# Optimization experiments

Measured on AMD Instinct MI355X. Metric: run time of the kernel, lower is better.

The kernel has to match this reference:

```python
import jax, jax.numpy as jnp
import numpy as np

B, N, C = 8, 4096, 256
HEADS = 8
DH = C // HEADS
SR = 4
EPS = 1e-5


def setup_inputs() -> dict:
    key = jax.random.key(0)
    ks = jax.random.split(key, 12)
    s = 0.02
    inp = {
        "x": jax.random.normal(ks[0], (B, N, C), dtype=jnp.float32),
        "H": 64,
        "W": 64,
        # nn.Linear weights stored torch-style [out, in]
        "q_w": jax.random.normal(ks[1], (C, C), dtype=jnp.float32) * s,
        "q_b": jax.random.normal(ks[2], (C,), dtype=jnp.float32) * s,
        "kv_w": jax.random.normal(ks[3], (2 * C, C), dtype=jnp.float32) * s,
        "kv_b": jax.random.normal(ks[4], (2 * C,), dtype=jnp.float32) * s,
        # Conv2d weight torch OIHW [C, C, SR, SR]
        "sr_w": jax.random.normal(ks[5], (C, C, SR, SR), dtype=jnp.float32) * s,
        "sr_b": jax.random.normal(ks[6], (C,), dtype=jnp.float32) * s,
        "ln_g": jnp.ones((C,), dtype=jnp.float32),
        "ln_b": jnp.zeros((C,), dtype=jnp.float32),
        "proj_w": jax.random.normal(ks[7], (C, C), dtype=jnp.float32) * s,
        "proj_b": jax.random.normal(ks[8], (C,), dtype=jnp.float32) * s,
    }
    return inp


def _layernorm(x, g, b):
    mu = jnp.mean(x, axis=-1, keepdims=True)
    var = jnp.mean(jnp.square(x - mu), axis=-1, keepdims=True)
    return (x - mu) * jax.lax.rsqrt(var + EPS) * g + b


def reference(x, H, W, q_w, q_b, kv_w, kv_b, sr_w, sr_b, ln_g, ln_b, proj_w, proj_b):
    b, n, c = x.shape
    scale = 1.0 / jnp.sqrt(jnp.float32(DH))

    # q projection -> [b, heads, n, dh]
    q = (x @ q_w.T + q_b).reshape(b, n, HEADS, DH).transpose(0, 2, 1, 3)

    # spatial reduction: conv stride=SR kernel=SR on the [b,H,W,c] image
    x_img = x.reshape(b, H, W, c)  # NHWC
    kern = jnp.transpose(sr_w, (2, 3, 1, 0))  # OIHW -> HWIO
    x_sr = jax.lax.conv_general_dilated(
        x_img, kern, window_strides=(SR, SR), padding="VALID",
        dimension_numbers=("NHWC", "HWIO", "NHWC")) + sr_b
    n_kv = (H // SR) * (W // SR)
    x_sr = x_sr.reshape(b, n_kv, c)
    x_sr = _layernorm(x_sr, ln_g, ln_b)

    # kv projection -> k, v: [b, heads, n_kv, dh]
    kv = (x_sr @ kv_w.T + kv_b).reshape(b, n_kv, 2, HEADS, DH)
    kv = kv.transpose(2, 0, 3, 1, 4)
    k, v = kv[0], kv[1]

    # attention (dropout rates are 0.0 / eval mode)
    attn = jnp.einsum("bhnd,bhmd->bhnm", q, k) * scale
    attn = jax.nn.softmax(attn, axis=-1)
    out = jnp.einsum("bhnm,bhmd->bhnd", attn, v)
    out = out.transpose(0, 2, 1, 3).reshape(b, n, c)
    return out @ proj_w.T + proj_b
```

## Files before the change

kernel.cpp:

```cpp
#include <hip/hip_runtime.h>

typedef unsigned short u16;
typedef float f32x4 __attribute__((ext_vector_type(4)));
typedef __bf16 bf16x4 __attribute__((ext_vector_type(4)));
typedef __bf16 bf16x8 __attribute__((ext_vector_type(8)));

#define B_ 8
#define N_ 4096
#define C_ 256
#define NKV 256
#define CEXP 0.25506604f

__device__ inline u16 f2bf(float f) {
    union { float f; unsigned u; } v; v.f = f;
    unsigned r = v.u + 0x7FFF + ((v.u >> 16) & 1);
    return (u16)(r >> 16);
}

__device__ inline void gload16(const void* g, void* l) {
    __builtin_amdgcn_global_load_lds(
        (const __attribute__((address_space(1))) void*)g,
        (__attribute__((address_space(3))) void*)l, 16, 0, 0);
}

__global__ __launch_bounds__(256) void prep_all(
    const float* __restrict__ x, u16* __restrict__ xb,
    const float* __restrict__ qw, const float* __restrict__ kvw,
    const float* __restrict__ pw, const float* __restrict__ srw,
    u16* __restrict__ wqb, u16* __restrict__ wkv, u16* __restrict__ wp, u16* __restrict__ wsr)
{
    size_t base = ((size_t)blockIdx.x * 256 + threadIdx.x) * 4;
    float4 v = *(const float4*)(x + base);
    ushort4 o;
    o.x = f2bf(v.x); o.y = f2bf(v.y); o.z = f2bf(v.z); o.w = f2bf(v.w);
    *(ushort4*)(xb + base) = o;

    int t = blockIdx.x * 256 + threadIdx.x;
    int stride = gridDim.x * 256;
    for (int i = t; i < 65536; i += stride) { wqb[i] = f2bf(qw[i]); wp[i] = f2bf(pw[i]); }
    for (int i = t; i < 131072; i += stride) wkv[i] = f2bf(kvw[i]);
    for (int i = t; i < 1048576; i += stride) {
        int oo = i >> 12, kk = i & 4095;
        int ci = kk & 255, khkw = kk >> 8;
        wsr[i] = f2bf(srw[(size_t)(oo * 256 + ci) * 16 + khkw]);
    }
}

template<int OUTMODE, bool SCALEK, bool IM2COL>
__device__ __forceinline__ void gemm_body(
    u16* As, u16* Bs,
    const u16* __restrict__ A, const u16* __restrict__ Bt,
    const float* __restrict__ bias, void* __restrict__ outp,
    int M, int Nn, int K, int kchunk, int bm, int bn, int bz)
{
    const int tid = threadIdx.x;
    const int k0 = bz * kchunk;
    const int wid = tid >> 6, lane = tid & 63;
    const int wr = wid >> 1, wc = wid & 1;
    const int lrow = lane & 15, lkg = lane >> 4;

    f32x4 acc[4][4] = {};

    const int c1 = tid, c2 = tid + 256;
    const int r1 = c1 >> 2, cl1 = (c1 & 3) * 8;
    const int r2 = c2 >> 2, cl2 = (c2 & 3) * 8;
    const u16 *aS1, *aS2;
    if constexpr (IM2COL) {
        const int g1 = bm * 128 + r1, g2 = bm * 128 + r2;
        const int b1 = g1 >> 8, p1 = g1 & 255;
        const int b2 = g2 >> 8, p2 = g2 & 255;
        aS1 = A + ((size_t)(b1 * 4096 + (p1 >> 4) * 256 + (p1 & 15) * 4) * 256 + cl1);
        aS2 = A + ((size_t)(b2 * 4096 + (p2 >> 4) * 256 + (p2 & 15) * 4) * 256 + cl2);
    } else {
        aS1 = A + (size_t)(bm * 128 + r1) * K + k0 + cl1;
        aS2 = A + (size_t)(bm * 128 + r2) * K + k0 + cl2;
    }
    const u16* bS1 = Bt + (size_t)(bn * 128 + r1) * K + k0 + cl1;
    const u16* bS2 = Bt + (size_t)(bn * 128 + r2) * K + k0 + cl2;
    u16* aD1 = As + c1 * 8;  u16* aD2 = As + c2 * 8;
    u16* bD1 = Bs + c1 * 8;  u16* bD2 = Bs + c2 * 8;

    for (int kk = 0; kk < kchunk; kk += 32) {
        int aoff;
        if constexpr (IM2COL) {
            const int K0 = k0 + kk;
            const int khkw = K0 >> 8;
            aoff = ((khkw >> 2) * 64 + (khkw & 3)) * 256 + (K0 & 255);
        } else {
            aoff = kk;
        }
        gload16(aS1 + aoff, aD1);
        gload16(aS2 + aoff, aD2);
        gload16(bS1 + kk, bD1);
        gload16(bS2 + kk, bD2);
        __syncthreads();
        bf16x8 af[4], bff[4];
#pragma unroll
        for (int i = 0; i < 4; ++i) {
            af[i]  = *(const bf16x8*)(As + (wr * 64 + i * 16 + lrow) * 32 + lkg * 8);
            bff[i] = *(const bf16x8*)(Bs + (wc * 64 + i * 16 + lrow) * 32 + lkg * 8);
        }
#pragma unroll
        for (int i = 0; i < 4; ++i)
#pragma unroll
            for (int j = 0; j < 4; ++j)
                acc[i][j] = __builtin_amdgcn_mfma_f32_16x16x32_bf16(af[i], bff[j], acc[i][j], 0, 0, 0);
        __syncthreads();
    }

    const int row0 = bm * 128 + wr * 64;
    const int col0 = bn * 128 + wc * 64;
    if constexpr (OUTMODE == 2) {
        float* o = (float*)outp + (size_t)bz * M * Nn;
#pragma unroll
        for (int i = 0; i < 4; ++i)
#pragma unroll
            for (int j = 0; j < 4; ++j)
#pragma unroll
                for (int reg = 0; reg < 4; ++reg)
                    o[(size_t)(row0 + i * 16 + lkg * 4 + reg) * Nn + col0 + j * 16 + lrow] = acc[i][j][reg];
    } else {
#pragma unroll
        for (int j = 0; j < 4; ++j) {
            const int col = col0 + j * 16 + lrow;
            float bv = bias[col];
            float sc = 1.0f;
            if constexpr (SCALEK) { if (col < 256) sc = CEXP; }
#pragma unroll
            for (int i = 0; i < 4; ++i)
#pragma unroll
                for (int reg = 0; reg < 4; ++reg) {
                    const size_t idx = (size_t)(row0 + i * 16 + lkg * 4 + reg) * Nn + col;
                    const float val = (acc[i][j][reg] + bv) * sc;
                    if constexpr (OUTMODE == 1) ((u16*)outp)[idx] = f2bf(val);
                    else                        ((float*)outp)[idx] = val;
                }
        }
    }
}

template<int OUTMODE, bool SCALEK, bool IM2COL>
__global__ __launch_bounds__(256, 2) void gemm128(
    const u16* __restrict__ A, const u16* __restrict__ Bt,
    const float* __restrict__ bias, void* __restrict__ outp,
    int M, int Nn, int K, int kchunk)
{
    __shared__ __align__(16) u16 As[128 * 32];
    __shared__ __align__(16) u16 Bs[128 * 32];
    gemm_body<OUTMODE, SCALEK, IM2COL>(As, Bs, A, Bt, bias, outp, M, Nn, K, kchunk,
                                       blockIdx.x, blockIdx.y, blockIdx.z);
}

__global__ __launch_bounds__(256, 2) void fused_convq(
    const u16* __restrict__ xb, const u16* __restrict__ wsr, float* __restrict__ part,
    const u16* __restrict__ wqb, const float* __restrict__ qb, u16* __restrict__ qbuf)
{
    __shared__ __align__(16) u16 As[128 * 32];
    __shared__ __align__(16) u16 Bs[128 * 32];
    const int id = blockIdx.x;
    if (id < 128) {
        const int z = id & 3, t = id >> 2;
        gemm_body<2, false, true>(As, Bs, xb, wsr, nullptr, part,
                                  2048, 256, 4096, 1024, t >> 1, t & 1, z);
    } else {
        const int qid = id - 128;
        gemm_body<1, false, false>(As, Bs, xb, wqb, qb, qbuf,
                                   32768, 256, 256, 256, qid >> 1, qid & 1, 0);
    }
}

__global__ __launch_bounds__(256) void ln_kernel(
    const float* __restrict__ part, const float* __restrict__ srb,
    const float* __restrict__ g, const float* __restrict__ bb, u16* __restrict__ out)
{
    const int row = blockIdx.x, c = threadIdx.x;
    const size_t idx = (size_t)row * 256 + c;
    float v = srb[c];
#pragma unroll
    for (int z = 0; z < 4; ++z) v += part[idx + (size_t)z * 524288];
    float s = v;
#pragma unroll
    for (int m = 1; m < 64; m <<= 1) s += __shfl_xor(s, m);
    __shared__ float red[4];
    if ((c & 63) == 0) red[c >> 6] = s;
    __syncthreads();
    float tot = red[0] + red[1] + red[2] + red[3];
    float mu = tot * (1.0f / 256.0f);
    float d = v - mu;
    float s2 = d * d;
#pragma unroll
    for (int m = 1; m < 64; m <<= 1) s2 += __shfl_xor(s2, m);
    __syncthreads();
    if ((c & 63) == 0) red[c >> 6] = s2;
    __syncthreads();
    float var = (red[0] + red[1] + red[2] + red[3]) * (1.0f / 256.0f);
    out[idx] = f2bf(d * rsqrtf(var + 1e-5f) * g[c] + bb[c]);
}

__global__ __launch_bounds__(256, 4) void attn_kernel(
    const u16* __restrict__ qbuf, const u16* __restrict__ kvbuf, u16* __restrict__ obuf)
{
    __shared__ __align__(16) u16 Ks[256 * 32];
    __shared__ __align__(16) u16 Vt[32 * 264];
    const int qt = blockIdx.x, h = blockIdx.y, b = blockIdx.z;
    const int tid = threadIdx.x;
    const int wid = tid >> 6, lane = tid & 63;
    const int lrow = lane & 15, lkg = lane >> 4;

    {
        const int rsub = lane >> 2, piece = lane & 3;
#pragma unroll
        for (int i = 0; i < 4; ++i) {
            const int c = wid * 4 + i;
            const u16* src = kvbuf + (size_t)(b * 256 + c * 16 + rsub) * 512 + h * 32 + piece * 8;
            gload16(src, Ks + c * 512 + lane * 8);
        }
    }
    {
        const int i = tid & 127, dbase = (tid >> 7) * 16;
        const u16* vs0 = kvbuf + (size_t)(b * 256 + 2 * i) * 512 + 256 + h * 32 + dbase;
        const u16* vs1 = vs0 + 512;
        ushort4 a0 = *(const ushort4*)(vs0);
        ushort4 a1 = *(const ushort4*)(vs0 + 4);
        ushort4 a2 = *(const ushort4*)(vs0 + 8);
        ushort4 a3 = *(const ushort4*)(vs0 + 12);
        ushort4 b0 = *(const ushort4*)(vs1);
        ushort4 b1 = *(const ushort4*)(vs1 + 4);
        ushort4 b2 = *(const ushort4*)(vs1 + 8);
        ushort4 b3 = *(const ushort4*)(vs1 + 12);
        unsigned* vw = (unsigned*)(Vt + (size_t)dbase * 264 + 2 * i);
#define VPACK(d, lo, hi) vw[(d) * 132] = ((unsigned)(hi) << 16) | (lo)
        VPACK(0,  a0.x, b0.x); VPACK(1,  a0.y, b0.y); VPACK(2,  a0.z, b0.z); VPACK(3,  a0.w, b0.w);
        VPACK(4,  a1.x, b1.x); VPACK(5,  a1.y, b1.y); VPACK(6,  a1.z, b1.z); VPACK(7,  a1.w, b1.w);
        VPACK(8,  a2.x, b2.x); VPACK(9,  a2.y, b2.y); VPACK(10, a2.z, b2.z); VPACK(11, a2.w, b2.w);
        VPACK(12, a3.x, b3.x); VPACK(13, a3.y, b3.y); VPACK(14, a3.z, b3.z); VPACK(15, a3.w, b3.w);
#undef VPACK
    }

    const int qcol = h * 32 + lkg * 8;
    bf16x8 qf = *(const bf16x8*)(qbuf +
        (size_t)(b * 4096 + qt * 64 + wid * 16 + lrow) * 256 + qcol);

    bf16x8 onesf = {};
    if (lrow == 0) {
#pragma unroll
        for (int e = 0; e < 8; ++e) onesf[e] = (__bf16)1.0f;
    }

    __syncthreads();

    f32x4 acc[16];
#pragma unroll
    for (int nf = 0; nf < 16; ++nf) acc[nf] = (f32x4){0.f, 0.f, 0.f, 0.f};
#pragma unroll
    for (int nf = 0; nf < 16; ++nf) {
        bf16x8 kfr = *(const bf16x8*)(Ks + (nf * 16 + lrow) * 32 + lkg * 8);
        acc[nf] = __builtin_amdgcn_mfma_f32_16x16x32_bf16(kfr, qf, acc[nf], 0, 0, 0);
    }

    bf16x8 pa8[8];
#pragma unroll
    for (int nf2 = 0; nf2 < 8; ++nf2) {
        bf16x8 pv;
#pragma unroll
        for (int half = 0; half < 2; ++half) {
#pragma unroll
            for (int r = 0; r < 4; ++r)
                pv[half * 4 + r] = (__bf16)exp2f(acc[2 * nf2 + half][r]);
        }
        pa8[nf2] = pv;
    }

    f32x4 o0 = (f32x4){0.f, 0.f, 0.f, 0.f};
    f32x4 o1 = (f32x4){0.f, 0.f, 0.f, 0.f};
    f32x4 o2 = (f32x4){0.f, 0.f, 0.f, 0.f};
#pragma unroll
    for (int nf2 = 0; nf2 < 8; ++nf2) {
        bf16x4 lo0 = *(const bf16x4*)(Vt + lrow * 264 + nf2 * 32 + lkg * 4);
        bf16x4 hi0 = *(const bf16x4*)(Vt + lrow * 264 + nf2 * 32 + 16 + lkg * 4);
        bf16x4 lo1 = *(const bf16x4*)(Vt + (16 + lrow) * 264 + nf2 * 32 + lkg * 4);
        bf16x4 hi1 = *(const bf16x4*)(Vt + (16 + lrow) * 264 + nf2 * 32 + 16 + lkg * 4);
        bf16x8 v0 = __builtin_shufflevector(lo0, hi0, 0, 1, 2, 3, 4, 5, 6, 7);
        bf16x8 v1 = __builtin_shufflevector(lo1, hi1, 0, 1, 2, 3, 4, 5, 6, 7);
        o0 = __builtin_amdgcn_mfma_f32_16x16x32_bf16(pa8[nf2], v0, o0, 0, 0, 0);
        o1 = __builtin_amdgcn_mfma_f32_16x16x32_bf16(pa8[nf2], v1, o1, 0, 0, 0);
        o2 = __builtin_amdgcn_mfma_f32_16x16x32_bf16(pa8[nf2], onesf, o2, 0, 0, 0);
    }

    float invq[4];
#pragma unroll
    for (int r = 0; r < 4; ++r)
        invq[r] = __shfl(__builtin_amdgcn_rcpf(o2[r]), lane & 48);

    const size_t obase = (size_t)(b * 4096 + qt * 64 + wid * 16);
#pragma unroll
    for (int r = 0; r < 4; ++r) {
        u16* op = obuf + (obase + lkg * 4 + r) * 256 + h * 32 + lrow;
        op[0]  = f2bf(o0[r] * invq[r]);
        op[16] = f2bf(o1[r] * invq[r]);
    }
}

extern "C" void kernel_launch(void* const* d_in, const int* in_sizes, int n_in,
                              void* d_out, int out_size, void* d_ws, size_t ws_size,
                              hipStream_t stream)
{
    (void)in_sizes; (void)n_in; (void)out_size; (void)ws_size;
    const float* x   = (const float*)d_in[0];
    const float* qw  = (const float*)d_in[3];
    const float* qb  = (const float*)d_in[4];
    const float* kvw = (const float*)d_in[5];
    const float* kvb = (const float*)d_in[6];
    const float* srw = (const float*)d_in[7];
    const float* srb = (const float*)d_in[8];
    const float* lng = (const float*)d_in[9];
    const float* lnb = (const float*)d_in[10];
    const float* pw  = (const float*)d_in[11];
    const float* pb  = (const float*)d_in[12];

    char* ws = (char*)d_ws;
    u16*   xb      = (u16*)(ws + 0);
    u16*   att     = (u16*)(ws + 16777216);
    float* part    = (float*)(ws + 33554432);
    u16*   wsr     = (u16*)(ws + 50331648);
    u16*   wqb     = (u16*)(ws + 52428800);
    u16*   wkvb    = (u16*)(ws + 52559872);
    u16*   wpb     = (u16*)(ws + 52822016);
    u16*   xsr     = (u16*)(ws + 52953088);
    u16*   kvo     = (u16*)(ws + 54001664);
    u16*   qbuf    = (u16*)d_out;

    prep_all<<<8192, 256, 0, stream>>>(x, xb, qw, kvw, pw, srw, wqb, wkvb, wpb, wsr);
    fused_convq<<<640, 256, 0, stream>>>(xb, wsr, part, wqb, qb, qbuf);
    ln_kernel<<<2048, 256, 0, stream>>>(part, srb, lng, lnb, xsr);
    gemm128<1, true,  false><<<dim3(16, 4, 1), 256, 0, stream>>>(xsr, wkvb, kvb, kvo, 2048, 512, 256, 256);
    attn_kernel<<<dim3(64, 8, 8), 256, 0, stream>>>(qbuf, kvo, att);
    gemm128<0, false, false><<<dim3(256, 2, 1), 256, 0, stream>>>(att, wpb, pb, d_out, 32768, 256, 256, 256);
}
```

Measured before the change: 94.06 us.

## Fuse layernorm into conv/q kernel via atomic counter, smaller KV GEMM, swizzle K LDS

Removes the separate layernorm launch. The last 128 q-projection blocks of the fused conv/q kernel spin on a global counter until all conv split-K blocks finish, then reduce the partials and apply layernorm. The KV projection gets a dedicated 64x64-tile GEMM with more blocks, to fill the GPU better than the 64-block 128-tile version. The attention K tile in LDS is XOR-swizzled to reduce bank conflicts. The spin-wait relies on the conv blocks being scheduled before the waiting blocks, which risks deadlock or stalls if block scheduling order differs.

```diff
diff --git a/kernel.cpp b/kernel.cpp
--- a/kernel.cpp
+++ b/kernel.cpp
@@ -27,8 +27,11 @@
     const float* __restrict__ x, u16* __restrict__ xb,
     const float* __restrict__ qw, const float* __restrict__ kvw,
     const float* __restrict__ pw, const float* __restrict__ srw,
-    u16* __restrict__ wqb, u16* __restrict__ wkv, u16* __restrict__ wp, u16* __restrict__ wsr)
-{
+    u16* __restrict__ wqb, u16* __restrict__ wkv, u16* __restrict__ wp, u16* __restrict__ wsr,
+    int* __restrict__ ctr)
+{
+    if (blockIdx.x == 0 && threadIdx.x == 0) ctr[0] = 0;
+
     size_t base = ((size_t)blockIdx.x * 256 + threadIdx.x) * 4;
     float4 v = *(const float4*)(x + base);
     ushort4 o;
@@ -46,7 +49,7 @@
     }
 }
 
-template<int OUTMODE, bool SCALEK, bool IM2COL>
+template<int OUTMODE, bool IM2COL>
 __device__ __forceinline__ void gemm_body(
     u16* As, u16* Bs,
     const u16* __restrict__ A, const u16* __restrict__ Bt,
@@ -124,14 +127,12 @@
         for (int j = 0; j < 4; ++j) {
             const int col = col0 + j * 16 + lrow;
             float bv = bias[col];
-            float sc = 1.0f;
-            if constexpr (SCALEK) { if (col < 256) sc = CEXP; }
 #pragma unroll
             for (int i = 0; i < 4; ++i)
 #pragma unroll
                 for (int reg = 0; reg < 4; ++reg) {
                     const size_t idx = (size_t)(row0 + i * 16 + lkg * 4 + reg) * Nn + col;
-                    const float val = (acc[i][j][reg] + bv) * sc;
+                    const float val = acc[i][j][reg] + bv;
                     if constexpr (OUTMODE == 1) ((u16*)outp)[idx] = f2bf(val);
                     else                        ((float*)outp)[idx] = val;
                 }
@@ -139,7 +140,7 @@
     }
 }
 
-template<int OUTMODE, bool SCALEK, bool IM2COL>
+template<int OUTMODE, bool IM2COL>
 __global__ __launch_bounds__(256, 2) void gemm128(
     const u16* __restrict__ A, const u16* __restrict__ Bt,
     const float* __restrict__ bias, void* __restrict__ outp,
@@ -147,54 +148,121 @@
 {
     __shared__ __align__(16) u16 As[128 * 32];
     __shared__ __align__(16) u16 Bs[128 * 32];
-    gemm_body<OUTMODE, SCALEK, IM2COL>(As, Bs, A, Bt, bias, outp, M, Nn, K, kchunk,
-                                       blockIdx.x, blockIdx.y, blockIdx.z);
+    gemm_body<OUTMODE, IM2COL>(As, Bs, A, Bt, bias, outp, M, Nn, K, kchunk,
+                               blockIdx.x, blockIdx.y, blockIdx.z);
+}
+
+__global__ __launch_bounds__(256, 2) void gemm64_kv(
+    const u16* __restrict__ A, const u16* __restrict__ Bt,
+    const float* __restrict__ bias, u16* __restrict__ outp)
+{
+    __shared__ __align__(16) u16 As[64 * 32];
+    __shared__ __align__(16) u16 Bs[64 * 32];
+    const int tid = threadIdx.x, bm = blockIdx.x, bn = blockIdx.y;
+    const int wid = tid >> 6, lane = tid & 63;
+    const int wr = wid >> 1, wc = wid & 1;
+    const int lrow = lane & 15, lkg = lane >> 4;
+
+    f32x4 acc[2][2] = {};
+    const int r = tid >> 2, cl = (tid & 3) * 8;
+    const u16* aS = A  + (size_t)(bm * 64 + r) * 256 + cl;
+    const u16* bS = Bt + (size_t)(bn * 64 + r) * 256 + cl;
+    u16* aD = As + tid * 8;
+    u16* bD = Bs + tid * 8;
+
+    for (int kk = 0; kk < 256; kk += 32) {
+        gload16(aS + kk, aD);
+        gload16(bS + kk, bD);
+        __syncthreads();
+        bf16x8 af[2], bf2[2];
+#pragma unroll
+        for (int i = 0; i < 2; ++i) {
+            af[i]  = *(const bf16x8*)(As + (wr * 32 + i * 16 + lrow) * 32 + lkg * 8);
+            bf2[i] = *(const bf16x8*)(Bs + (wc * 32 + i * 16 + lrow) * 32 + lkg * 8);
+        }
+#pragma unroll
+        for (int i = 0; i < 2; ++i)
+#pragma unroll
+            for (int j = 0; j < 2; ++j)
+                acc[i][j] = __builtin_amdgcn_mfma_f32_16x16x32_bf16(af[i], bf2[j], acc[i][j], 0, 0, 0);
+        __syncthreads();
+    }
+
+    const int row0 = bm * 64 + wr * 32;
+    const int col0 = bn * 64 + wc * 32;
+#pragma unroll
+    for (int j = 0; j < 2; ++j) {
+        const int col = col0 + j * 16 + lrow;
+        const float bv = bias[col];
+        const float sc = (col < 256) ? CEXP : 1.0f;
+#pragma unroll
+        for (int i = 0; i < 2; ++i)
+#pragma unroll
+            for (int reg = 0; reg < 4; ++reg)
+                outp[(size_t)(row0 + i * 16 + lkg * 4 + reg) * 512 + col] =
+                    f2bf((acc[i][j][reg] + bv) * sc);
+    }
 }
 
 __global__ __launch_bounds__(256, 2) void fused_convq(
     const u16* __restrict__ xb, const u16* __restrict__ wsr, float* __restrict__ part,
-    const u16* __restrict__ wqb, const float* __restrict__ qb, u16* __restrict__ qbuf)
+    const u16* __restrict__ wqb, const float* __restrict__ qb, u16* __restrict__ qbuf,
+    const float* __restrict__ srb, const float* __restrict__ lng, const float* __restrict__ lnb,
+    u16* __restrict__ xsr, int* __restrict__ ctr)
 {
     __shared__ __align__(16) u16 As[128 * 32];
     __shared__ __align__(16) u16 Bs[128 * 32];
     const int id = blockIdx.x;
     if (id < 128) {
         const int z = id & 3, t = id >> 2;
-        gemm_body<2, false, true>(As, Bs, xb, wsr, nullptr, part,
-                                  2048, 256, 4096, 1024, t >> 1, t & 1, z);
+        gemm_body<2, true>(As, Bs, xb, wsr, nullptr, part,
+                           2048, 256, 4096, 1024, t >> 1, t & 1, z);
+        __syncthreads();
+        if (threadIdx.x == 0) { __threadfence(); atomicAdd(ctr, 1); }
     } else {
         const int qid = id - 128;
-        gemm_body<1, false, false>(As, Bs, xb, wqb, qb, qbuf,
-                                   32768, 256, 256, 256, qid >> 1, qid & 1, 0);
-    }
-}
-
-__global__ __launch_bounds__(256) void ln_kernel(
-    const float* __restrict__ part, const float* __restrict__ srb,
-    const float* __restrict__ g, const float* __restrict__ bb, u16* __restrict__ out)
-{
-    const int row = blockIdx.x, c = threadIdx.x;
-    const size_t idx = (size_t)row * 256 + c;
-    float v = srb[c];
-#pragma unroll
-    for (int z = 0; z < 4; ++z) v += part[idx + (size_t)z * 524288];
-    float s = v;
-#pragma unroll
-    for (int m = 1; m < 64; m <<= 1) s += __shfl_xor(s, m);
-    __shared__ float red[4];
-    if ((c & 63) == 0) red[c >> 6] = s;
-    __syncthreads();
-    float tot = red[0] + red[1] + red[2] + red[3];
-    float mu = tot * (1.0f / 256.0f);
-    float d = v - mu;
-    float s2 = d * d;
-#pragma unroll
-    for (int m = 1; m < 64; m <<= 1) s2 += __shfl_xor(s2, m);
-    __syncthreads();
-    if ((c & 63) == 0) red[c >> 6] = s2;
-    __syncthreads();
-    float var = (red[0] + red[1] + red[2] + red[3]) * (1.0f / 256.0f);
-    out[idx] = f2bf(d * rsqrtf(var + 1e-5f) * g[c] + bb[c]);
+        gemm_body<1, false>(As, Bs, xb, wqb, qb, qbuf,
+                            32768, 256, 256, 256, qid >> 1, qid & 1, 0);
+        if (id >= 512) {
+            if (threadIdx.x == 0) {
+                while (atomicAdd(ctr, 0) < 128) __builtin_amdgcn_s_sleep(8);
+            }
+            __syncthreads();
+            __threadfence();
+            const int lane = threadIdx.x & 63;
+            const int wv = threadIdx.x >> 6;
+            const int col = lane * 4;
+            const float4 gv = *(const float4*)(lng + col);
+            const float4 bv = *(const float4*)(lnb + col);
+            const float4 sb = *(const float4*)(srb + col);
+            const int rbase = (id - 512) * 16 + wv * 4;
+            for (int rr = 0; rr < 4; ++rr) {
+                const int row = rbase + rr;
+                const float* pr = part + (size_t)row * 256 + col;
+                float vx = sb.x, vy = sb.y, vz = sb.z, vw = sb.w;
+#pragma unroll
+                for (int z = 0; z < 4; ++z) {
+                    float4 p = *(const float4*)(pr + (size_t)z * 524288);
+                    vx += p.x; vy += p.y; vz += p.z; vw += p.w;
+                }
+                float s = vx + vy + vz + vw;
+#pragma unroll
+                for (int m = 1; m < 64; m <<= 1) s += __shfl_xor(s, m);
+                const float mu = s * (1.0f / 256.0f);
+                const float dx = vx - mu, dy = vy - mu, dz = vz - mu, dw = vw - mu;
+                float s2 = dx * dx + dy * dy + dz * dz + dw * dw;
+#pragma unroll
+                for (int m = 1; m < 64; m <<= 1) s2 += __shfl_xor(s2, m);
+                const float rs = rsqrtf(s2 * (1.0f / 256.0f) + 1e-5f);
+                ushort4 o;
+                o.x = f2bf(dx * rs * gv.x + bv.x);
+                o.y = f2bf(dy * rs * gv.y + bv.y);
+                o.z = f2bf(dz * rs * gv.z + bv.z);
+                o.w = f2bf(dw * rs * gv.w + bv.w);
+                *(ushort4*)(xsr + (size_t)row * 256 + col) = o;
+            }
+        }
+    }
 }
 
 __global__ __launch_bounds__(256, 4) void attn_kernel(
@@ -208,12 +276,13 @@
     const int lrow = lane & 15, lkg = lane >> 4;
 
     {
-        const int rsub = lane >> 2, piece = lane & 3;
+        const int loff = (lane * 16) ^ (((lane >> 3) & 7) << 4);
+        const int rloc = loff >> 6, piece = (loff >> 4) & 3;
 #pragma unroll
         for (int i = 0; i < 4; ++i) {
             const int c = wid * 4 + i;
-            const u16* src = kvbuf + (size_t)(b * 256 + c * 16 + rsub) * 512 + h * 32 + piece * 8;
-            gload16(src, Ks + c * 512 + lane * 8);
+            const u16* src = kvbuf + (size_t)(b * 256 + c * 16 + rloc) * 512 + h * 32 + piece * 8;
+            gload16(src, Ks + c * 512);
         }
     }
     {
@@ -249,12 +318,13 @@
 
     __syncthreads();
 
+    const int pbase = (lrow * 64 + lkg * 16) ^ (((lrow >> 1) & 7) << 4);
     f32x4 acc[16];
 #pragma unroll
     for (int nf = 0; nf < 16; ++nf) acc[nf] = (f32x4){0.f, 0.f, 0.f, 0.f};
 #pragma unroll
     for (int nf = 0; nf < 16; ++nf) {
-        bf16x8 kfr = *(const bf16x8*)(Ks + (nf * 16 + lrow) * 32 + lkg * 8);
+        bf16x8 kfr = *(const bf16x8*)((const char*)Ks + pbase + nf * 1024);
         acc[nf] = __builtin_amdgcn_mfma_f32_16x16x32_bf16(kfr, qf, acc[nf], 0, 0, 0);
     }
 
@@ -328,12 +398,13 @@
     u16*   wpb     = (u16*)(ws + 52822016);
     u16*   xsr     = (u16*)(ws + 52953088);
     u16*   kvo     = (u16*)(ws + 54001664);
+    int*   ctr     = (int*)(ws + 56098816);
     u16*   qbuf    = (u16*)d_out;
 
-    prep_all<<<8192, 256, 0, stream>>>(x, xb, qw, kvw, pw, srw, wqb, wkvb, wpb, wsr);
-    fused_convq<<<640, 256, 0, stream>>>(xb, wsr, part, wqb, qb, qbuf);
-    ln_kernel<<<2048, 256, 0, stream>>>(part, srb, lng, lnb, xsr);
-    gemm128<1, true,  false><<<dim3(16, 4, 1), 256, 0, stream>>>(xsr, wkvb, kvb, kvo, 2048, 512, 256, 256);
+    prep_all<<<8192, 256, 0, stream>>>(x, xb, qw, kvw, pw, srw, wqb, wkvb, wpb, wsr, ctr);
+    fused_convq<<<640, 256, 0, stream>>>(xb, wsr, part, wqb, qb, qbuf,
+                                         srb, lng, lnb, xsr, ctr);
+    gemm64_kv<<<dim3(32, 8), 256, 0, stream>>>(xsr, wkvb, kvb, kvo);
     attn_kernel<<<dim3(64, 8, 8), 256, 0, stream>>>(qbuf, kvo, att);
-    gemm128<0, false, false><<<dim3(256, 2, 1), 256, 0, stream>>>(att, wpb, pb, d_out, 32768, 256, 256, 256);
-}
+    gemm128<0, false><<<dim3(256, 2, 1), 256, 0, stream>>>(att, wpb, pb, d_out, 32768, 256, 256, 256);
+}
```

New measurement: 108.5 us. 1.15x slower.
